# Optimization experiments

Measured on AMD Instinct MI355X. Metric: run time of the kernel, lower is better.

## Reference

```python
import jax, jax.numpy as jnp
import numpy as np

HEADS = 16
DIM_HEAD = 64
SCALE = DIM_HEAD ** -0.5


def setup_inputs() -> dict:
    key = jax.random.key(0)
    ks = jax.random.split(key, 7)
    b, n, m, d = 2, 2048, 2048, 1024
    inner = HEADS * DIM_HEAD  # 1024
    patch_embed = jax.random.normal(ks[0], (b, n, d), dtype=jnp.float32)
    pixel_embed = jax.random.normal(ks[1], (b, m, d), dtype=jnp.float32)
    s = 1.0 / np.sqrt(d)
    Wq = jax.random.normal(ks[2], (d, inner), dtype=jnp.float32) * s
    Wk = jax.random.normal(ks[3], (d, inner), dtype=jnp.float32) * s
    Wv = jax.random.normal(ks[4], (d, inner), dtype=jnp.float32) * s
    Wo = jax.random.normal(ks[5], (inner, d), dtype=jnp.float32) * (1.0 / np.sqrt(inner))
    bo = jax.random.normal(ks[6], (d,), dtype=jnp.float32) * 0.01
    return {"patch_embed": patch_embed, "pixel_embed": pixel_embed,
            "Wq": Wq, "Wk": Wk, "Wv": Wv, "Wo": Wo, "bo": bo}


def reference(patch_embed, pixel_embed, Wq, Wk, Wv, Wo, bo):
    b, n, _ = patch_embed.shape
    h, dh = HEADS, DIM_HEAD
    # projections
    q = patch_embed @ Wq  # [b, n, h*dh]
    k = pixel_embed @ Wk  # [b, m, h*dh]
    v = pixel_embed @ Wv  # [b, m, h*dh]
    # split heads: [b, seq, h, dh]
    q = q.reshape(b, n, h, dh)
    k = k.reshape(b, -1, h, dh)
    v = v.reshape(b, -1, h, dh)
    sim = jnp.einsum('bihd,bjhd->bhij', q, k) * SCALE  # [b, h, n, m]
    attn = jax.nn.softmax(sim, axis=-1)
    out = jnp.einsum('bhij,bjhd->bihd', attn, v)  # [b, n, h, dh]
    out = out.reshape(b, n, h * dh)
    return out @ Wo + bo  # [b, n, query_dim]
```

## Files before the change

kernel.cpp:

```cpp
#include <hip/hip_runtime.h>

#define SEQ 2048
#define DMODEL 1024
#define HEADS 16
#define DH 64
#define QSCALE 0.180336880f

typedef __attribute__((ext_vector_type(8))) short short8;
typedef __attribute__((ext_vector_type(4))) float f32x4;

__device__ __forceinline__ ushort f2bf(float x) {
  union { float f; unsigned u; } v; v.f = x;
  return (ushort)((v.u + 0x7fffu + ((v.u >> 16) & 1u)) >> 16);
}

__device__ __forceinline__ void gld16(const ushort* g, ushort* l) {
  __builtin_amdgcn_global_load_lds(
      (const __attribute__((address_space(1))) unsigned int*)g,
      (__attribute__((address_space(3))) unsigned int*)l, 16, 0, 0);
}

__device__ __forceinline__ size_t qk_idx(int bh, int s, int d) {
  return ((((size_t)bh * (SEQ / 16) + (s >> 4)) * 2 + (d >> 5)) * 64 +
          ((d >> 3) & 3) * 16 + (s & 15)) * 8 + (d & 7);
}
__device__ __forceinline__ size_t v_idx(int bh, int s, int d) {
  return ((((size_t)bh * 4 + (d >> 4)) * (SEQ / 32) + (s >> 5)) * 64 +
          ((s >> 3) & 3) * 16 + (d & 15)) * 8 + (s & 7);
}

__global__ __launch_bounds__(256) void prologue(
    const float* __restrict__ patch, const float* __restrict__ pixel,
    const float* __restrict__ W0, const float* __restrict__ W1,
    const float* __restrict__ W2, const float* __restrict__ W3,
    ushort* __restrict__ pb, ushort* __restrict__ xb,
    ushort* __restrict__ O0, ushort* __restrict__ O1,
    ushort* __restrict__ O2, ushort* __restrict__ O3) {
  const int z = blockIdx.z;
  const int tx = threadIdx.x, ty = threadIdx.y;
  if (z < 2) {
    const float4* in = (const float4*)(z ? pixel : patch);
    ushort4* out = (ushort4*)(z ? xb : pb);
    const int base = (blockIdx.y * 32 + blockIdx.x) * 256 + ty * 32 + tx;
#pragma unroll
    for (int rep = 0; rep < 4; ++rep) {
      const int i = base + rep * 262144;
      float4 f = in[i];
      out[i] = make_ushort4(f2bf(f.x), f2bf(f.y), f2bf(f.z), f2bf(f.w));
    }
    return;
  }
  __shared__ float tile[32][33];
  const int zz = z - 2;
  const float* in = zz == 0 ? W0 : zz == 1 ? W1 : zz == 2 ? W2 : W3;
  ushort* out = zz == 0 ? O0 : zz == 1 ? O1 : zz == 2 ? O2 : O3;
  const float scale = zz == 0 ? QSCALE : 1.0f;
  const int n0 = blockIdx.x * 32, k0 = blockIdx.y * 32;
#pragma unroll
  for (int i = 0; i < 4; ++i)
    tile[ty + i * 8][tx] = in[(size_t)(k0 + ty + i * 8) * DMODEL + n0 + tx];
  __syncthreads();
#pragma unroll
  for (int i = 0; i < 4; ++i)
    out[(size_t)(n0 + ty + i * 8) * DMODEL + k0 + tx] =
        f2bf(tile[tx][ty + i * 8] * scale);
}

__global__ __launch_bounds__(256) void mfma_gemm_qkv(
    const ushort* __restrict__ pb, const ushort* __restrict__ xb,
    const ushort* __restrict__ wqt, const ushort* __restrict__ wkt,
    const ushort* __restrict__ wvt, ushort* __restrict__ qws,
    ushort* __restrict__ kws, ushort* __restrict__ vws) {
  __shared__ __align__(16) ushort As[128 * 64];
  __shared__ __align__(16) ushort Bs[128 * 64];
  const int z = blockIdx.z;
  const ushort* A = (z == 0) ? pb : xb;
  const ushort* Bt = (z == 0) ? wqt : (z == 1) ? wkt : wvt;

  const int t = threadIdx.x;
  const int w = t >> 6, lane = t & 63, ln = lane & 15, q = lane >> 4;
  const int wm = w & 1, wn = w >> 1;
  const int row0 = blockIdx.y * 128, col0 = blockIdx.x * 128;
  const int sw = ln & 7;

  f32x4 acc[4][4];
#pragma unroll
  for (int i = 0; i < 4; ++i)
#pragma unroll
    for (int j = 0; j < 4; ++j) acc[i][j] = (f32x4){0.f, 0.f, 0.f, 0.f};

  for (int k0 = 0; k0 < DMODEL; k0 += 64) {
    __syncthreads();
#pragma unroll
    for (int rep = 0; rep < 4; ++rep) {
      const int u0 = rep * 256 + w * 64;
      const int u = u0 + lane;
      const int r = u >> 3, gl = (u & 7) ^ (r & 7);
      gld16(&A[(size_t)(row0 + r) * DMODEL + k0 + gl * 8], &As[u0 * 8]);
      gld16(&Bt[(size_t)(col0 + r) * DMODEL + k0 + gl * 8], &Bs[u0 * 8]);
    }
    __syncthreads();
#pragma unroll
    for (int ks = 0; ks < 2; ++ks) {
      short8 af[4], bf[4];
#pragma unroll
      for (int rt = 0; rt < 4; ++rt)
        af[rt] = *(const short8*)&As[(wm * 64 + rt * 16 + ln) * 64 +
                                     (((ks * 4 + q) ^ sw) * 8)];
#pragma unroll
      for (int ct = 0; ct < 4; ++ct)
        bf[ct] = *(const short8*)&Bs[(wn * 64 + ct * 16 + ln) * 64 +
                                     (((ks * 4 + q) ^ sw) * 8)];
#pragma unroll
      for (int rt = 0; rt < 4; ++rt)
#pragma unroll
        for (int ct = 0; ct < 4; ++ct)
          acc[rt][ct] = __builtin_amdgcn_mfma_f32_16x16x32_bf16(af[rt], bf[ct],
                                                                acc[rt][ct], 0, 0, 0);
    }
  }

  if (z < 2) {
    ushort* dst = z == 0 ? qws : kws;
#pragma unroll
    for (int rt = 0; rt < 4; ++rt)
#pragma unroll
      for (int ct = 0; ct < 4; ++ct) {
        const int c = col0 + wn * 64 + ct * 16 + ln;
        const int h = c >> 6, d = c & 63;
#pragma unroll
        for (int reg = 0; reg < 4; ++reg) {
          const int r = row0 + wm * 64 + rt * 16 + q * 4 + reg;
          const int b = r >> 11, s = r & (SEQ - 1);
          dst[qk_idx(b * HEADS + h, s, d)] = f2bf(acc[rt][ct][reg]);
        }
      }
  } else {
#pragma unroll
    for (int rt = 0; rt < 4; ++rt)
#pragma unroll
      for (int ct = 0; ct < 4; ++ct) {
        const int c = col0 + wn * 64 + ct * 16 + ln;
        const int h = c >> 6, d = c & 63;
        const int r0 = row0 + wm * 64 + rt * 16 + q * 4;
        const int b = r0 >> 11, s0 = r0 & (SEQ - 1);
        ushort4 u4 = make_ushort4(f2bf(acc[rt][ct][0]), f2bf(acc[rt][ct][1]),
                                  f2bf(acc[rt][ct][2]), f2bf(acc[rt][ct][3]));
        *(ushort4*)&vws[v_idx(b * HEADS + h, s0, d)] = u4;
      }
  }
}

__global__ __launch_bounds__(256, 3) void flash_mfma(
    const ushort* __restrict__ Qg, const ushort* __restrict__ Kg,
    const ushort* __restrict__ Vg, ushort* __restrict__ Og) {
  __shared__ __align__(16) ushort Kst[2][8 * 512];
  __shared__ __align__(16) ushort Vst[2][8 * 512];
  __shared__ __align__(16) ushort Ps[128 * 72];

  const int t = threadIdx.x;
  const int w = t >> 6, lane = t & 63, ln = lane & 15, q = lane >> 4;
  const int bh = blockIdx.x;
  const int qt = blockIdx.y;

  const ushort* qg = Qg + (size_t)bh * SEQ * DH;
  const ushort* kg = Kg + (size_t)bh * SEQ * DH;
  const ushort* vg = Vg + (size_t)bh * DH * SEQ;

  short8 qf[2][2];
#pragma unroll
  for (int rt = 0; rt < 2; ++rt)
#pragma unroll
    for (int ks = 0; ks < 2; ++ks)
      qf[rt][ks] = *(const short8*)
          &qg[(((size_t)(qt * 8 + w * 2 + rt) * 2 + ks) * 64 + lane) * 8];

  float l_i[2][4];
  f32x4 acc_o[2][4];
#pragma unroll
  for (int rt = 0; rt < 2; ++rt)
#pragma unroll
    for (int reg = 0; reg < 4; ++reg) l_i[rt][reg] = 0.f;
#pragma unroll
  for (int rt = 0; rt < 2; ++rt)
#pragma unroll
    for (int nt = 0; nt < 4; ++nt) acc_o[rt][nt] = (f32x4){0.f, 0.f, 0.f, 0.f};

#pragma unroll
  for (int i = 0; i < 4; ++i) {
    const int f = w * 4 + i;
    if (f < 8) {
      gld16(&kg[(size_t)(0 * 8 + f) * 512 + lane * 8], &Kst[0][f * 512]);
    } else {
      const int f2 = f - 8, nt = f2 >> 1, ks2 = f2 & 1;
      gld16(&vg[(size_t)(nt * (SEQ / 32) + 0 * 2 + ks2) * 512 + lane * 8],
            &Vst[0][f2 * 512]);
    }
  }
  __syncthreads();

  for (int kt = 0; kt < SEQ / 64; ++kt) {
    const int cur = kt & 1;
    if (kt + 1 < SEQ / 64) {
      const int nxt = cur ^ 1;
#pragma unroll
      for (int i = 0; i < 4; ++i) {
        const int f = w * 4 + i;
        if (f < 8) {
          gld16(&kg[(size_t)((kt + 1) * 8 + f) * 512 + lane * 8],
                &Kst[nxt][f * 512]);
        } else {
          const int f2 = f - 8, nt = f2 >> 1, ks2 = f2 & 1;
          gld16(&vg[(size_t)(nt * (SEQ / 32) + (kt + 1) * 2 + ks2) * 512 +
                    lane * 8],
                &Vst[nxt][f2 * 512]);
        }
      }
    }

    f32x4 accs[2][4];
#pragma unroll
    for (int rt = 0; rt < 2; ++rt)
#pragma unroll
      for (int ct = 0; ct < 4; ++ct) accs[rt][ct] = (f32x4){0.f, 0.f, 0.f, 0.f};
#pragma unroll
    for (int ks = 0; ks < 2; ++ks)
#pragma unroll
      for (int ct = 0; ct < 4; ++ct) {
        const short8 bf = *(const short8*)&Kst[cur][(ct * 2 + ks) * 512 + lane * 8];
#pragma unroll
        for (int rt = 0; rt < 2; ++rt)
          accs[rt][ct] = __builtin_amdgcn_mfma_f32_16x16x32_bf16(
              qf[rt][ks], bf, accs[rt][ct], 0, 0, 0);
      }

#pragma unroll
    for (int rt = 0; rt < 2; ++rt)
#pragma unroll
      for (int ct = 0; ct < 4; ++ct)
#pragma unroll
        for (int reg = 0; reg < 4; ++reg) {
          const float p = __builtin_amdgcn_exp2f(accs[rt][ct][reg]);
          l_i[rt][reg] += p;
          union { float f; unsigned u; } v; v.f = p;
          Ps[(w * 32 + rt * 16 + q * 4 + reg) * 72 + ct * 16 + ln] =
              (ushort)((v.u + 0x8000u) >> 16);
        }

#pragma unroll
    for (int ks2 = 0; ks2 < 2; ++ks2) {
      short8 pa[2];
#pragma unroll
      for (int rt = 0; rt < 2; ++rt)
        pa[rt] = *(const short8*)&Ps[(w * 32 + rt * 16 + ln) * 72 +
                                     ks2 * 32 + q * 8];
#pragma unroll
      for (int nt = 0; nt < 4; ++nt) {
        const short8 bv = *(const short8*)&Vst[cur][(nt * 2 + ks2) * 512 + lane * 8];
#pragma unroll
        for (int rt = 0; rt < 2; ++rt)
          acc_o[rt][nt] = __builtin_amdgcn_mfma_f32_16x16x32_bf16(
              pa[rt], bv, acc_o[rt][nt], 0, 0, 0);
      }
    }

    __syncthreads();
  }

  const int b = bh >> 4, h = bh & 15;
#pragma unroll
  for (int rt = 0; rt < 2; ++rt)
#pragma unroll
    for (int reg = 0; reg < 4; ++reg) {
      float l = l_i[rt][reg];
      l += __shfl_xor(l, 1, 16);
      l += __shfl_xor(l, 2, 16);
      l += __shfl_xor(l, 4, 16);
      l += __shfl_xor(l, 8, 16);
      const float inv = 1.0f / l;
      const int s = qt * 128 + w * 32 + rt * 16 + q * 4 + reg;
#pragma unroll
      for (int nt = 0; nt < 4; ++nt)
        Og[(size_t)(b * SEQ + s) * DMODEL + h * DH + nt * 16 + ln] =
            f2bf(acc_o[rt][nt][reg] * inv);
    }
}

__global__ __launch_bounds__(256) void mfma_gemm_out(const ushort* __restrict__ A,
                                                     const ushort* __restrict__ Bt,
                                                     const float* __restrict__ bias,
                                                     float* __restrict__ dst) {
  __shared__ __align__(16) ushort As[64 * 64];
  __shared__ __align__(16) ushort Bs[128 * 64];
  const int t = threadIdx.x;
  const int w = t >> 6, lane = t & 63, ln = lane & 15, q = lane >> 4;
  const int wm = w & 1, wn = w >> 1;
  const int row0 = blockIdx.y * 64, col0 = blockIdx.x * 128;
  const int sw = ln & 7;

  f32x4 acc[2][4];
#pragma unroll
  for (int i = 0; i < 2; ++i)
#pragma unroll
    for (int j = 0; j < 4; ++j) acc[i][j] = (f32x4){0.f, 0.f, 0.f, 0.f};

  for (int k0 = 0; k0 < DMODEL; k0 += 64) {
    __syncthreads();
#pragma unroll
    for (int rep = 0; rep < 2; ++rep) {
      const int u0 = rep * 256 + w * 64;
      const int u = u0 + lane;
      const int r = u >> 3, gl = (u & 7) ^ (r & 7);
      gld16(&A[(size_t)(row0 + r) * DMODEL + k0 + gl * 8], &As[u0 * 8]);
    }
#pragma unroll
    for (int rep = 0; rep < 4; ++rep) {
      const int u0 = rep * 256 + w * 64;
      const int u = u0 + lane;
      const int r = u >> 3, gl = (u & 7) ^ (r & 7);
      gld16(&Bt[(size_t)(col0 + r) * DMODEL + k0 + gl * 8], &Bs[u0 * 8]);
    }
    __syncthreads();
#pragma unroll
    for (int ks = 0; ks < 2; ++ks) {
      short8 af[2], bf[4];
#pragma unroll
      for (int rt = 0; rt < 2; ++rt)
        af[rt] = *(const short8*)&As[(wm * 32 + rt * 16 + ln) * 64 +
                                     (((ks * 4 + q) ^ sw) * 8)];
#pragma unroll
      for (int ct = 0; ct < 4; ++ct)
        bf[ct] = *(const short8*)&Bs[(wn * 64 + ct * 16 + ln) * 64 +
                                     (((ks * 4 + q) ^ sw) * 8)];
#pragma unroll
      for (int rt = 0; rt < 2; ++rt)
#pragma unroll
        for (int ct = 0; ct < 4; ++ct)
          acc[rt][ct] = __builtin_amdgcn_mfma_f32_16x16x32_bf16(af[rt], bf[ct],
                                                                acc[rt][ct], 0, 0, 0);
    }
  }

#pragma unroll
  for (int rt = 0; rt < 2; ++rt)
#pragma unroll
    for (int ct = 0; ct < 4; ++ct) {
      const int c = col0 + wn * 64 + ct * 16 + ln;
      const float bi = bias[c];
#pragma unroll
      for (int reg = 0; reg < 4; ++reg) {
        const int r = row0 + wm * 32 + rt * 16 + q * 4 + reg;
        dst[(size_t)r * DMODEL + c] = acc[rt][ct][reg] + bi;
      }
    }
}

extern "C" void kernel_launch(void* const* d_in, const int* in_sizes, int n_in,
                              void* d_out, int out_size, void* d_ws,
                              size_t ws_size, hipStream_t stream) {
  const float* patch = (const float*)d_in[0];
  const float* pixel = (const float*)d_in[1];
  const float* Wq = (const float*)d_in[2];
  const float* Wk = (const float*)d_in[3];
  const float* Wv = (const float*)d_in[4];
  const float* Wo = (const float*)d_in[5];
  const float* bo = (const float*)d_in[6];
  float* out = (float*)d_out;

  const size_t E = (size_t)2 * SEQ * DMODEL;
  const size_t W = (size_t)DMODEL * DMODEL;
  ushort* pb  = (ushort*)d_ws;
  ushort* xb  = pb + E;
  ushort* wqt = xb + E;
  ushort* wkt = wqt + W;
  ushort* wvt = wkt + W;
  ushort* wot = wvt + W;
  ushort* qws = wot + W;
  ushort* kws = qws + E;
  ushort* vws = kws + E;
  ushort* aws = vws + E;

  prologue<<<dim3(32, 32, 6), dim3(32, 8), 0, stream>>>(
      patch, pixel, Wq, Wk, Wv, Wo, pb, xb, wqt, wkt, wvt, wot);
  mfma_gemm_qkv<<<dim3(8, 32, 3), 256, 0, stream>>>(pb, xb, wqt, wkt, wvt,
                                                    qws, kws, vws);
  flash_mfma<<<dim3(32, 16), 256, 0, stream>>>(qws, kws, vws, aws);
  mfma_gemm_out<<<dim3(8, 64), 256, 0, stream>>>(aws, wot, bo, out);
}
```

Measured before the change: 201.0 us.

## Shrink flash query tile to 64 rows and load V fragments directly from global

The attention kernel now gives each wave 16 query rows instead of 32, which halves the block's query tile and doubles the grid to 1024 blocks. V is no longer staged in shared memory: the V workspace layout is reordered so each key tile's fragments are contiguous, and every wave reads its V MFMA operands straight from global memory into registers. Less shared memory and fewer registers let the occupancy hint rise from 3 to 4 blocks. The trade-off is that K and V are reused across fewer query rows, so total K/V traffic doubles, and V reads now go through cache instead of LDS, with each wave loading the same V data separately.

```diff
diff --git a/kernel.cpp b/kernel.cpp
--- a/kernel.cpp
+++ b/kernel.cpp
@@ -25,7 +25,7 @@
           ((d >> 3) & 3) * 16 + (s & 15)) * 8 + (d & 7);
 }
 __device__ __forceinline__ size_t v_idx(int bh, int s, int d) {
-  return ((((size_t)bh * 4 + (d >> 4)) * (SEQ / 32) + (s >> 5)) * 64 +
+  return ((((size_t)bh * (SEQ / 32) + (s >> 5)) * 4 + (d >> 4)) * 64 +
           ((s >> 3) & 3) * 16 + (d & 15)) * 8 + (s & 7);
 }
 
@@ -151,12 +151,11 @@
   }
 }
 
-__global__ __launch_bounds__(256, 3) void flash_mfma(
+__global__ __launch_bounds__(256, 4) void flash_mfma(
     const ushort* __restrict__ Qg, const ushort* __restrict__ Kg,
     const ushort* __restrict__ Vg, ushort* __restrict__ Og) {
   __shared__ __align__(16) ushort Kst[2][8 * 512];
-  __shared__ __align__(16) ushort Vst[2][8 * 512];
-  __shared__ __align__(16) ushort Ps[128 * 72];
+  __shared__ __align__(16) ushort Ps[64 * 76];
 
   const int t = threadIdx.x;
   const int w = t >> 6, lane = t & 63, ln = lane & 15, q = lane >> 4;
@@ -167,101 +166,73 @@
   const ushort* kg = Kg + (size_t)bh * SEQ * DH;
   const ushort* vg = Vg + (size_t)bh * DH * SEQ;
 
-  short8 qf[2][2];
-#pragma unroll
-  for (int rt = 0; rt < 2; ++rt)
-#pragma unroll
-    for (int ks = 0; ks < 2; ++ks)
-      qf[rt][ks] = *(const short8*)
-          &qg[(((size_t)(qt * 8 + w * 2 + rt) * 2 + ks) * 64 + lane) * 8];
-
-  float l_i[2][4];
-  f32x4 acc_o[2][4];
-#pragma unroll
-  for (int rt = 0; rt < 2; ++rt)
-#pragma unroll
-    for (int reg = 0; reg < 4; ++reg) l_i[rt][reg] = 0.f;
-#pragma unroll
-  for (int rt = 0; rt < 2; ++rt)
-#pragma unroll
-    for (int nt = 0; nt < 4; ++nt) acc_o[rt][nt] = (f32x4){0.f, 0.f, 0.f, 0.f};
-
-#pragma unroll
-  for (int i = 0; i < 4; ++i) {
-    const int f = w * 4 + i;
-    if (f < 8) {
-      gld16(&kg[(size_t)(0 * 8 + f) * 512 + lane * 8], &Kst[0][f * 512]);
-    } else {
-      const int f2 = f - 8, nt = f2 >> 1, ks2 = f2 & 1;
-      gld16(&vg[(size_t)(nt * (SEQ / 32) + 0 * 2 + ks2) * 512 + lane * 8],
-            &Vst[0][f2 * 512]);
-    }
+  short8 qf[2];
+#pragma unroll
+  for (int ks = 0; ks < 2; ++ks)
+    qf[ks] = *(const short8*)
+        &qg[(((size_t)(qt * 4 + w) * 2 + ks) * 64 + lane) * 8];
+
+  float l_i[4] = {0.f, 0.f, 0.f, 0.f};
+  f32x4 acc_o[4];
+#pragma unroll
+  for (int nt = 0; nt < 4; ++nt) acc_o[nt] = (f32x4){0.f, 0.f, 0.f, 0.f};
+
+#pragma unroll
+  for (int i = 0; i < 2; ++i) {
+    const int f = w * 2 + i;
+    gld16(&kg[(size_t)f * 512 + lane * 8], &Kst[0][f * 512]);
   }
   __syncthreads();
 
   for (int kt = 0; kt < SEQ / 64; ++kt) {
     const int cur = kt & 1;
     if (kt + 1 < SEQ / 64) {
-      const int nxt = cur ^ 1;
-#pragma unroll
-      for (int i = 0; i < 4; ++i) {
-        const int f = w * 4 + i;
-        if (f < 8) {
-          gld16(&kg[(size_t)((kt + 1) * 8 + f) * 512 + lane * 8],
-                &Kst[nxt][f * 512]);
-        } else {
-          const int f2 = f - 8, nt = f2 >> 1, ks2 = f2 & 1;
-          gld16(&vg[(size_t)(nt * (SEQ / 32) + (kt + 1) * 2 + ks2) * 512 +
-                    lane * 8],
-                &Vst[nxt][f2 * 512]);
-        }
-      }
-    }
-
-    f32x4 accs[2][4];
-#pragma unroll
-    for (int rt = 0; rt < 2; ++rt)
-#pragma unroll
-      for (int ct = 0; ct < 4; ++ct) accs[rt][ct] = (f32x4){0.f, 0.f, 0.f, 0.f};
+#pragma unroll
+      for (int i = 0; i < 2; ++i) {
+        const int f = w * 2 + i;
+        gld16(&kg[(size_t)((kt + 1) * 8 + f) * 512 + lane * 8],
+              &Kst[cur ^ 1][f * 512]);
+      }
+    }
+
+    short8 bv[2][4];
+#pragma unroll
+    for (int ks2 = 0; ks2 < 2; ++ks2)
+#pragma unroll
+      for (int nt = 0; nt < 4; ++nt)
+        bv[ks2][nt] = *(const short8*)
+            &vg[((size_t)((kt * 2 + ks2) * 4 + nt) * 64 + lane) * 8];
+
+    f32x4 accs[4];
+#pragma unroll
+    for (int ct = 0; ct < 4; ++ct) accs[ct] = (f32x4){0.f, 0.f, 0.f, 0.f};
 #pragma unroll
     for (int ks = 0; ks < 2; ++ks)
 #pragma unroll
       for (int ct = 0; ct < 4; ++ct) {
-        const short8 bf = *(const short8*)&Kst[cur][(ct * 2 + ks) * 512 + lane * 8];
-#pragma unroll
-        for (int rt = 0; rt < 2; ++rt)
-          accs[rt][ct] = __builtin_amdgcn_mfma_f32_16x16x32_bf16(
-              qf[rt][ks], bf, accs[rt][ct], 0, 0, 0);
-      }
-
-#pragma unroll
-    for (int rt = 0; rt < 2; ++rt)
-#pragma unroll
-      for (int ct = 0; ct < 4; ++ct)
-#pragma unroll
-        for (int reg = 0; reg < 4; ++reg) {
-          const float p = __builtin_amdgcn_exp2f(accs[rt][ct][reg]);
-          l_i[rt][reg] += p;
-          union { float f; unsigned u; } v; v.f = p;
-          Ps[(w * 32 + rt * 16 + q * 4 + reg) * 72 + ct * 16 + ln] =
-              (ushort)((v.u + 0x8000u) >> 16);
-        }
+        const short8 bfr = *(const short8*)&Kst[cur][(ct * 2 + ks) * 512 + lane * 8];
+        accs[ct] = __builtin_amdgcn_mfma_f32_16x16x32_bf16(
+            qf[ks], bfr, accs[ct], 0, 0, 0);
+      }
+
+#pragma unroll
+    for (int ct = 0; ct < 4; ++ct)
+#pragma unroll
+      for (int reg = 0; reg < 4; ++reg) {
+        const float p = __builtin_amdgcn_exp2f(accs[ct][reg]);
+        l_i[reg] += p;
+        union { float f; unsigned u; } v; v.f = p;
+        Ps[(w * 16 + q * 4 + reg) * 76 + ct * 16 + ln] =
+            (ushort)((v.u + 0x8000u) >> 16);
+      }
 
 #pragma unroll
     for (int ks2 = 0; ks2 < 2; ++ks2) {
-      short8 pa[2];
-#pragma unroll
-      for (int rt = 0; rt < 2; ++rt)
-        pa[rt] = *(const short8*)&Ps[(w * 32 + rt * 16 + ln) * 72 +
-                                     ks2 * 32 + q * 8];
-#pragma unroll
-      for (int nt = 0; nt < 4; ++nt) {
-        const short8 bv = *(const short8*)&Vst[cur][(nt * 2 + ks2) * 512 + lane * 8];
-#pragma unroll
-        for (int rt = 0; rt < 2; ++rt)
-          acc_o[rt][nt] = __builtin_amdgcn_mfma_f32_16x16x32_bf16(
-              pa[rt], bv, acc_o[rt][nt], 0, 0, 0);
-      }
+      const short8 pa = *(const short8*)&Ps[(w * 16 + ln) * 76 + ks2 * 32 + q * 8];
+#pragma unroll
+      for (int nt = 0; nt < 4; ++nt)
+        acc_o[nt] = __builtin_amdgcn_mfma_f32_16x16x32_bf16(
+            pa, bv[ks2][nt], acc_o[nt], 0, 0, 0);
     }
 
     __syncthreads();
@@ -269,21 +240,19 @@
 
   const int b = bh >> 4, h = bh & 15;
 #pragma unroll
-  for (int rt = 0; rt < 2; ++rt)
-#pragma unroll
-    for (int reg = 0; reg < 4; ++reg) {
-      float l = l_i[rt][reg];
-      l += __shfl_xor(l, 1, 16);
-      l += __shfl_xor(l, 2, 16);
-      l += __shfl_xor(l, 4, 16);
-      l += __shfl_xor(l, 8, 16);
-      const float inv = 1.0f / l;
-      const int s = qt * 128 + w * 32 + rt * 16 + q * 4 + reg;
-#pragma unroll
-      for (int nt = 0; nt < 4; ++nt)
-        Og[(size_t)(b * SEQ + s) * DMODEL + h * DH + nt * 16 + ln] =
-            f2bf(acc_o[rt][nt][reg] * inv);
-    }
+  for (int reg = 0; reg < 4; ++reg) {
+    float l = l_i[reg];
+    l += __shfl_xor(l, 1, 16);
+    l += __shfl_xor(l, 2, 16);
+    l += __shfl_xor(l, 4, 16);
+    l += __shfl_xor(l, 8, 16);
+    const float inv = 1.0f / l;
+    const int s = qt * 64 + w * 16 + q * 4 + reg;
+#pragma unroll
+    for (int nt = 0; nt < 4; ++nt)
+      Og[(size_t)(b * SEQ + s) * DMODEL + h * DH + nt * 16 + ln] =
+          f2bf(acc_o[nt][reg] * inv);
+  }
 }
 
 __global__ __launch_bounds__(256) void mfma_gemm_out(const ushort* __restrict__ A,
@@ -384,6 +353,6 @@
       patch, pixel, Wq, Wk, Wv, Wo, pb, xb, wqt, wkt, wvt, wot);
   mfma_gemm_qkv<<<dim3(8, 32, 3), 256, 0, stream>>>(pb, xb, wqt, wkt, wvt,
                                                     qws, kws, vws);
-  flash_mfma<<<dim3(32, 16), 256, 0, stream>>>(qws, kws, vws, aws);
+  flash_mfma<<<dim3(32, 32), 256, 0, stream>>>(qws, kws, vws, aws);
   mfma_gemm_out<<<dim3(8, 64), 256, 0, stream>>>(aws, wot, bo, out);
 }
```

Result: slower. 208.1 us (+3.5%).
